# Kernel optimization log

Hardware: AMD Instinct MI355X
Metric: run time of the kernel (lower is better)

## Reference

```python
import jax, jax.numpy as jnp
import numpy as np

# Module hyperparams (from init_kwargs)
VX, VY = 0.16, 0.16
PC_RANGE = (0.0, -39.68, -3.0, 69.12, 39.68, 1.0)
X_OFFSET = VX / 2 + PC_RANGE[0]
Y_OFFSET = VY / 2 + PC_RANGE[1]
X_L = int((PC_RANGE[3] - PC_RANGE[0]) / VX)  # 432
Y_L = int((PC_RANGE[4] - PC_RANGE[1]) / VY)  # 496
IN_CH, OUT_CH = 9, 64
BN_EPS = 1e-3
P, N_MAX, B = 40000, 32, 4


def setup_inputs() -> dict:
    key = jax.random.key(0)
    k1, k2, k3 = jax.random.split(key, 3)
    pillars = jax.random.normal(k1, (P, N_MAX, 4), dtype=jnp.float32)
    # Unique (per batch) pillar coordinates so the scatter is well-defined.
    rng = np.random.default_rng(0)
    per = P // B
    rows = []
    for b in range(B):
        lin = rng.choice(Y_L * X_L, size=per, replace=False)
        ys, xs = lin // X_L, lin % X_L
        rows.append(np.stack([np.full(per, b, np.int32), xs.astype(np.int32), ys.astype(np.int32)], axis=1))
    coors_batch = jnp.asarray(np.concatenate(rows, axis=0))  # (P,3): [b, x, y]
    npoints_per_pillar = jax.random.randint(k2, (P,), 1, N_MAX + 1, dtype=jnp.int32)
    # Learned params: 1x1 Conv1d weight (no bias) + BN affine
    W = jax.random.normal(k3, (OUT_CH, IN_CH), dtype=jnp.float32) * 0.1
    gamma = jnp.ones((OUT_CH,), dtype=jnp.float32)
    beta = jnp.zeros((OUT_CH,), dtype=jnp.float32)
    return {"pillars": pillars, "coors_batch": coors_batch,
            "npoints_per_pillar": npoints_per_pillar,
            "W": W, "gamma": gamma, "beta": beta, "batch_size": B}


def reference(pillars, coors_batch, npoints_per_pillar, W, gamma, beta, batch_size):
    npts = npoints_per_pillar.astype(pillars.dtype)
    # offset of each point from pillar mean (xyz)
    center = jnp.sum(pillars[:, :, :3], axis=1, keepdims=True) / npts[:, None, None]
    offset_pt_center = pillars[:, :, :3] - center                      # (P,N,3)
    cx = coors_batch[:, None, 1:2].astype(pillars.dtype) * VX + X_OFFSET
    cy = coors_batch[:, None, 2:3].astype(pillars.dtype) * VY + Y_OFFSET
    x_off = pillars[:, :, :1] - cx                                     # (P,N,1)
    y_off = pillars[:, :, 1:2] - cy                                    # (P,N,1)
    features = jnp.concatenate([pillars, offset_pt_center, x_off, y_off], axis=-1)  # (P,N,9)
    mask = (jnp.arange(N_MAX)[None, :] < npoints_per_pillar[:, None]).astype(features.dtype)
    features = features * mask[:, :, None]
    # 1x1 Conv1d == per-point channel mix -> (P, C_out, N)
    x = jnp.einsum('pnc,oc->pon', features, W)
    # BatchNorm1d (training-mode stats over pillar and point dims, biased var)
    mean = jnp.mean(x, axis=(0, 2))
    var = jnp.var(x, axis=(0, 2))
    x = gamma[None, :, None] * (x - mean[None, :, None]) * jax.lax.rsqrt(var[None, :, None] + BN_EPS) + beta[None, :, None]
    x = jax.nn.relu(x)
    pooled = jnp.max(x, axis=-1)                                       # (P, C_out)
    # Single vectorized scatter into BEV canvas: (B, Y, X, C) then -> (B, C, Y, X)
    canvas = jnp.zeros((batch_size, Y_L, X_L, OUT_CH), dtype=jnp.float32)
    canvas = canvas.at[coors_batch[:, 0], coors_batch[:, 2], coors_batch[:, 1]].set(pooled)
    return jnp.transpose(canvas, (0, 3, 1, 2))
```

## Files before the change

kernel.cpp:

```cpp
#include <hip/hip_runtime.h>
#include <math.h>

#define P_TOT 40000
#define NMAX 32
#define BATCH 4
#define YL 496
#define XL 432
#define CIN 9
#define COUT 64
#define NTRI 45
#define PN_F 1280000.0f

#define MAP_ELEMS (BATCH * YL * XL)
#define MAP_BYTES (MAP_ELEMS * 4)
#define STATS_OFF MAP_BYTES
#define SCALE_OFF (STATS_OFF + 256)
#define SHIFT_OFF (SCALE_OFF + 256)
#define POOLED_OFF (SHIFT_OFF + 256)

#define STATS_BLOCKS 256

__global__ __launch_bounds__(256) void k_init(int* __restrict__ map,
                                              float* __restrict__ stats) {
    int i = blockIdx.x * 256 + threadIdx.x;
    if (i < MAP_ELEMS) map[i] = -1;
    if (i < 54) stats[i] = 0.0f;
}

__global__ __launch_bounds__(256) void k_stats(const float4* __restrict__ pillars,
                                               const int* __restrict__ coors,
                                               const int* __restrict__ npp,
                                               int* __restrict__ map,
                                               float* __restrict__ stats) {
    const int wave = threadIdx.x >> 6;
    const int lane = threadIdx.x & 63;
    const int half = lane >> 5;
    const int n = lane & 31;
    const int gw = blockIdx.x * 4 + wave;
    const int totalWaves = STATS_BLOCKS * 4;

    float s1[CIN];
    float s2[NTRI];
#pragma unroll
    for (int i = 0; i < CIN; i++) s1[i] = 0.0f;
#pragma unroll
    for (int i = 0; i < NTRI; i++) s2[i] = 0.0f;

    for (int p0 = gw * 2; p0 < P_TOT; p0 += totalWaves * 2) {
        int p = p0 + half;
        float4 q = pillars[(size_t)p * NMAX + n];

        float sx = q.x, sy = q.y, sz = q.z;
#pragma unroll
        for (int off = 1; off < 32; off <<= 1) {
            sx += __shfl_xor(sx, off, 32);
            sy += __shfl_xor(sy, off, 32);
            sz += __shfl_xor(sz, off, 32);
        }
        int npts = npp[p];
        float fn = (float)npts;
        float mx = sx / fn, my = sy / fn, mz = sz / fn;

        int xi = coors[p * 3 + 1];
        int yi = coors[p * 3 + 2];
        if (n == 0) {
            int b = coors[p * 3 + 0];
            map[(b * YL + yi) * XL + xi] = p;
        }
        float cx = (float)xi * 0.16f + 0.08f;
        float cy = (float)yi * 0.16f + (-39.6f);

        float msk = (n < npts) ? 1.0f : 0.0f;
        float f[CIN];
        f[0] = q.x * msk; f[1] = q.y * msk; f[2] = q.z * msk; f[3] = q.w * msk;
        f[4] = (q.x - mx) * msk; f[5] = (q.y - my) * msk; f[6] = (q.z - mz) * msk;
        f[7] = (q.x - cx) * msk; f[8] = (q.y - cy) * msk;

        int k = 0;
#pragma unroll
        for (int a = 0; a < CIN; a++) {
            s1[a] += f[a];
#pragma unroll
            for (int c = a; c < CIN; c++) s2[k++] += f[a] * f[c];
        }
    }

#pragma unroll
    for (int i = 0; i < CIN; i++) {
        float v = s1[i];
        for (int off = 1; off < 64; off <<= 1) v += __shfl_xor(v, off, 64);
        s1[i] = v;
    }
#pragma unroll
    for (int i = 0; i < NTRI; i++) {
        float v = s2[i];
        for (int off = 1; off < 64; off <<= 1) v += __shfl_xor(v, off, 64);
        s2[i] = v;
    }

    __shared__ float red[4][54];
    if (lane == 0) {
#pragma unroll
        for (int i = 0; i < CIN; i++) red[wave][i] = s1[i];
#pragma unroll
        for (int i = 0; i < NTRI; i++) red[wave][CIN + i] = s2[i];
    }
    __syncthreads();
    if (threadIdx.x < 54) {
        float v = red[0][threadIdx.x] + red[1][threadIdx.x] +
                  red[2][threadIdx.x] + red[3][threadIdx.x];
        atomicAdd(&stats[threadIdx.x], v);
    }
}

__global__ void k_finalize(const float* __restrict__ W,
                           const float* __restrict__ gamma,
                           const float* __restrict__ beta,
                           const float* __restrict__ stats,
                           float* __restrict__ scale,
                           float* __restrict__ shift) {
    int o = threadIdx.x;
    float w[CIN];
#pragma unroll
    for (int c = 0; c < CIN; c++) w[c] = W[o * CIN + c];

    const float invPN = 1.0f / PN_F;
    float mu = 0.0f;
#pragma unroll
    for (int c = 0; c < CIN; c++) mu += w[c] * (stats[c] * invPN);

    float ex2 = 0.0f;
    int k = 0;
#pragma unroll
    for (int a = 0; a < CIN; a++) {
#pragma unroll
        for (int c = a; c < CIN; c++) {
            float Mv = stats[CIN + k] * invPN;
            float t = w[a] * w[c] * Mv;
            ex2 += (a == c) ? t : 2.0f * t;
            k++;
        }
    }
    float var = ex2 - mu * mu;
    float sc = gamma[o] * rsqrtf(var + 1e-3f);
    scale[o] = sc;
    shift[o] = beta[o] - mu * sc;
}

__global__ __launch_bounds__(256) void k_pool(const float4* __restrict__ pillars,
                                              const int* __restrict__ coors,
                                              const int* __restrict__ npp,
                                              const float* __restrict__ W,
                                              const float* __restrict__ scale,
                                              const float* __restrict__ shift,
                                              float* __restrict__ pooled) {
    __shared__ float fsh[4][NMAX][CIN];
    int w = threadIdx.x >> 6;
    int lane = threadIdx.x & 63;
    int p = blockIdx.x * 4 + w;
    int n = lane & 31;

    float4 q = pillars[(size_t)p * NMAX + n];
    float sx = q.x, sy = q.y, sz = q.z;
#pragma unroll
    for (int off = 1; off < 32; off <<= 1) {
        sx += __shfl_xor(sx, off, 32);
        sy += __shfl_xor(sy, off, 32);
        sz += __shfl_xor(sz, off, 32);
    }
    int npts = npp[p];
    float fn = (float)npts;
    float mx = sx / fn, my = sy / fn, mz = sz / fn;
    int xi = coors[p * 3 + 1];
    int yi = coors[p * 3 + 2];
    float cx = (float)xi * 0.16f + 0.08f;
    float cy = (float)yi * 0.16f + (-39.6f);

    if (lane < 32) {
        bool valid = (n < npts);
        fsh[w][n][0] = valid ? q.x : 0.0f;
        fsh[w][n][1] = valid ? q.y : 0.0f;
        fsh[w][n][2] = valid ? q.z : 0.0f;
        fsh[w][n][3] = valid ? q.w : 0.0f;
        fsh[w][n][4] = valid ? (q.x - mx) : 0.0f;
        fsh[w][n][5] = valid ? (q.y - my) : 0.0f;
        fsh[w][n][6] = valid ? (q.z - mz) : 0.0f;
        fsh[w][n][7] = valid ? (q.x - cx) : 0.0f;
        fsh[w][n][8] = valid ? (q.y - cy) : 0.0f;
    }
    __syncthreads();

    float wv[CIN];
#pragma unroll
    for (int c = 0; c < CIN; c++) wv[c] = W[lane * CIN + c];
    float sc = scale[lane];
    float sh = shift[lane];

    float m = -INFINITY;
#pragma unroll 4
    for (int nn = 0; nn < NMAX; nn++) {
        float d = 0.0f;
#pragma unroll
        for (int c = 0; c < CIN; c++) d += wv[c] * fsh[w][nn][c];
        m = fmaxf(m, sc * d + sh);
    }
    pooled[(size_t)p * COUT + lane] = fmaxf(m, 0.0f);
}

__global__ __launch_bounds__(256) void k_scatter(const int* __restrict__ map,
                                                 const float* __restrict__ pooled,
                                                 float* __restrict__ out) {
    int i = blockIdx.x * 256 + threadIdx.x;
    if (i >= BATCH * YL * (XL / 4)) return;
    int x4 = i % (XL / 4);
    int r = i / (XL / 4);
    int y = r % YL;
    int b = r / YL;

    const int4 pid = *(const int4*)(map + (size_t)(b * YL + y) * XL + x4 * 4);
    size_t obase = ((size_t)(b * COUT) * YL + y) * XL + (size_t)x4 * 4;
    const size_t cstride = (size_t)YL * XL;

    const float4 zero = make_float4(0.f, 0.f, 0.f, 0.f);
#pragma unroll 4
    for (int c4 = 0; c4 < COUT / 4; c4++) {
        float4 r0 = zero, r1 = zero, r2 = zero, r3 = zero;
        if (pid.x >= 0) r0 = *(const float4*)(pooled + (size_t)pid.x * COUT + c4 * 4);
        if (pid.y >= 0) r1 = *(const float4*)(pooled + (size_t)pid.y * COUT + c4 * 4);
        if (pid.z >= 0) r2 = *(const float4*)(pooled + (size_t)pid.z * COUT + c4 * 4);
        if (pid.w >= 0) r3 = *(const float4*)(pooled + (size_t)pid.w * COUT + c4 * 4);
        float* o0 = out + obase + (size_t)(c4 * 4) * cstride;
        *(float4*)(o0)               = make_float4(r0.x, r1.x, r2.x, r3.x);
        *(float4*)(o0 + cstride)     = make_float4(r0.y, r1.y, r2.y, r3.y);
        *(float4*)(o0 + 2 * cstride) = make_float4(r0.z, r1.z, r2.z, r3.z);
        *(float4*)(o0 + 3 * cstride) = make_float4(r0.w, r1.w, r2.w, r3.w);
    }
}

extern "C" void kernel_launch(void* const* d_in, const int* in_sizes, int n_in,
                              void* d_out, int out_size, void* d_ws, size_t ws_size,
                              hipStream_t stream) {
    const float4* pillars = (const float4*)d_in[0];
    const int* coors = (const int*)d_in[1];
    const int* npp = (const int*)d_in[2];
    const float* W = (const float*)d_in[3];
    const float* gamma = (const float*)d_in[4];
    const float* beta = (const float*)d_in[5];
    float* out = (float*)d_out;

    char* ws = (char*)d_ws;
    int* map = (int*)(ws);
    float* stats = (float*)(ws + STATS_OFF);
    float* scale = (float*)(ws + SCALE_OFF);
    float* shift = (float*)(ws + SHIFT_OFF);
    float* pooled = (float*)(ws + POOLED_OFF);

    k_init<<<(MAP_ELEMS + 255) / 256, 256, 0, stream>>>(map, stats);
    k_stats<<<STATS_BLOCKS, 256, 0, stream>>>(pillars, coors, npp, map, stats);
    k_finalize<<<1, 64, 0, stream>>>(W, gamma, beta, stats, scale, shift);
    k_pool<<<P_TOT / 4, 256, 0, stream>>>(pillars, coors, npp, W, scale, shift, pooled);
    k_scatter<<<(BATCH * YL * (XL / 4) + 255) / 256, 256, 0, stream>>>(map, pooled, out);
}
```

Before: 318.6 us.

## Fuse all stages into one cooperative persistent kernel with grid syncs

```diff
diff --git a/kernel.cpp b/kernel.cpp
--- a/kernel.cpp
+++ b/kernel.cpp
@@ -1,5 +1,8 @@
 #include <hip/hip_runtime.h>
+#include <hip/hip_cooperative_groups.h>
 #include <math.h>
+
+namespace cg = cooperative_groups;
 
 #define P_TOT 40000
 #define NMAX 32
@@ -18,222 +21,229 @@
 #define SHIFT_OFF (SCALE_OFF + 256)
 #define POOLED_OFF (SHIFT_OFF + 256)
 
-#define STATS_BLOCKS 256
-
-__global__ __launch_bounds__(256) void k_init(int* __restrict__ map,
-                                              float* __restrict__ stats) {
-    int i = blockIdx.x * 256 + threadIdx.x;
-    if (i < MAP_ELEMS) map[i] = -1;
-    if (i < 54) stats[i] = 0.0f;
-}
-
-__global__ __launch_bounds__(256) void k_stats(const float4* __restrict__ pillars,
-                                               const int* __restrict__ coors,
-                                               const int* __restrict__ npp,
-                                               int* __restrict__ map,
-                                               float* __restrict__ stats) {
-    const int wave = threadIdx.x >> 6;
-    const int lane = threadIdx.x & 63;
-    const int half = lane >> 5;
-    const int n = lane & 31;
-    const int gw = blockIdx.x * 4 + wave;
-    const int totalWaves = STATS_BLOCKS * 4;
-
-    float s1[CIN];
-    float s2[NTRI];
-#pragma unroll
-    for (int i = 0; i < CIN; i++) s1[i] = 0.0f;
-#pragma unroll
-    for (int i = 0; i < NTRI; i++) s2[i] = 0.0f;
-
-    for (int p0 = gw * 2; p0 < P_TOT; p0 += totalWaves * 2) {
-        int p = p0 + half;
-        float4 q = pillars[(size_t)p * NMAX + n];
-
-        float sx = q.x, sy = q.y, sz = q.z;
-#pragma unroll
-        for (int off = 1; off < 32; off <<= 1) {
-            sx += __shfl_xor(sx, off, 32);
-            sy += __shfl_xor(sy, off, 32);
-            sz += __shfl_xor(sz, off, 32);
-        }
-        int npts = npp[p];
-        float fn = (float)npts;
-        float mx = sx / fn, my = sy / fn, mz = sz / fn;
-
-        int xi = coors[p * 3 + 1];
-        int yi = coors[p * 3 + 2];
-        if (n == 0) {
-            int b = coors[p * 3 + 0];
-            map[(b * YL + yi) * XL + xi] = p;
-        }
-        float cx = (float)xi * 0.16f + 0.08f;
-        float cy = (float)yi * 0.16f + (-39.6f);
-
-        float msk = (n < npts) ? 1.0f : 0.0f;
-        float f[CIN];
-        f[0] = q.x * msk; f[1] = q.y * msk; f[2] = q.z * msk; f[3] = q.w * msk;
-        f[4] = (q.x - mx) * msk; f[5] = (q.y - my) * msk; f[6] = (q.z - mz) * msk;
-        f[7] = (q.x - cx) * msk; f[8] = (q.y - cy) * msk;
-
+#define GRID_MAX 1024
+#define NCELL4 (BATCH * YL * (XL / 4))
+
+__global__ __launch_bounds__(256, 4) void k_fused(
+        const float4* __restrict__ pillars,
+        const int* __restrict__ coors,
+        const int* __restrict__ npp,
+        const float* __restrict__ W,
+        const float* __restrict__ gamma,
+        const float* __restrict__ beta,
+        int* __restrict__ map,
+        float* __restrict__ stats,
+        float* __restrict__ scale,
+        float* __restrict__ shift,
+        float* __restrict__ pooled,
+        float* __restrict__ out,
+        int nblocks) {
+    cg::grid_group grid = cg::this_grid();
+    const int tid = threadIdx.x;
+    const int gtid = blockIdx.x * 256 + tid;
+    const int nthreads = nblocks * 256;
+    const int wave = tid >> 6;
+    const int lane = tid & 63;
+
+    __shared__ float red[4][54];
+    __shared__ float fsh[4][NMAX][CIN];
+
+    {
+        int4* m4 = (int4*)map;
+        const int4 neg1 = make_int4(-1, -1, -1, -1);
+        for (int i = gtid; i < MAP_ELEMS / 4; i += nthreads) m4[i] = neg1;
+        if (gtid < 54) stats[gtid] = 0.0f;
+    }
+    grid.sync();
+
+    {
+        const int half = lane >> 5;
+        const int n = lane & 31;
+        const int gw = blockIdx.x * 4 + wave;
+        const int totalWaves = nblocks * 4;
+
+        float s1[CIN];
+        float s2[NTRI];
+#pragma unroll
+        for (int i = 0; i < CIN; i++) s1[i] = 0.0f;
+#pragma unroll
+        for (int i = 0; i < NTRI; i++) s2[i] = 0.0f;
+
+        for (int p0 = gw * 2; p0 < P_TOT; p0 += totalWaves * 2) {
+            int p = p0 + half;
+            float4 q = pillars[(size_t)p * NMAX + n];
+
+            float sx = q.x, sy = q.y, sz = q.z;
+#pragma unroll
+            for (int off = 1; off < 32; off <<= 1) {
+                sx += __shfl_xor(sx, off, 32);
+                sy += __shfl_xor(sy, off, 32);
+                sz += __shfl_xor(sz, off, 32);
+            }
+            int npts = npp[p];
+            float fn = (float)npts;
+            float mx = sx / fn, my = sy / fn, mz = sz / fn;
+
+            int xi = coors[p * 3 + 1];
+            int yi = coors[p * 3 + 2];
+            if (n == 0) {
+                int b = coors[p * 3 + 0];
+                map[(b * YL + yi) * XL + xi] = p;
+            }
+            float cx = (float)xi * 0.16f + 0.08f;
+            float cy = (float)yi * 0.16f + (-39.6f);
+
+            float msk = (n < npts) ? 1.0f : 0.0f;
+            float f[CIN];
+            f[0] = q.x * msk; f[1] = q.y * msk; f[2] = q.z * msk; f[3] = q.w * msk;
+            f[4] = (q.x - mx) * msk; f[5] = (q.y - my) * msk; f[6] = (q.z - mz) * msk;
+            f[7] = (q.x - cx) * msk; f[8] = (q.y - cy) * msk;
+
+            int k = 0;
+#pragma unroll
+            for (int a = 0; a < CIN; a++) {
+                s1[a] += f[a];
+#pragma unroll
+                for (int c = a; c < CIN; c++) s2[k++] += f[a] * f[c];
+            }
+        }
+
+#pragma unroll
+        for (int i = 0; i < CIN; i++) {
+            float v = s1[i];
+            for (int off = 1; off < 64; off <<= 1) v += __shfl_xor(v, off, 64);
+            s1[i] = v;
+        }
+#pragma unroll
+        for (int i = 0; i < NTRI; i++) {
+            float v = s2[i];
+            for (int off = 1; off < 64; off <<= 1) v += __shfl_xor(v, off, 64);
+            s2[i] = v;
+        }
+        if (lane == 0) {
+#pragma unroll
+            for (int i = 0; i < CIN; i++) red[wave][i] = s1[i];
+#pragma unroll
+            for (int i = 0; i < NTRI; i++) red[wave][CIN + i] = s2[i];
+        }
+        __syncthreads();
+        if (tid < 54) {
+            float v = red[0][tid] + red[1][tid] + red[2][tid] + red[3][tid];
+            atomicAdd(&stats[tid], v);
+        }
+    }
+    grid.sync();
+
+    if (blockIdx.x == 0 && tid < COUT) {
+        int o = tid;
+        float w[CIN];
+#pragma unroll
+        for (int c = 0; c < CIN; c++) w[c] = W[o * CIN + c];
+
+        const float invPN = 1.0f / PN_F;
+        float mu = 0.0f;
+#pragma unroll
+        for (int c = 0; c < CIN; c++) mu += w[c] * (stats[c] * invPN);
+
+        float ex2 = 0.0f;
         int k = 0;
 #pragma unroll
         for (int a = 0; a < CIN; a++) {
-            s1[a] += f[a];
-#pragma unroll
-            for (int c = a; c < CIN; c++) s2[k++] += f[a] * f[c];
-        }
-    }
-
-#pragma unroll
-    for (int i = 0; i < CIN; i++) {
-        float v = s1[i];
-        for (int off = 1; off < 64; off <<= 1) v += __shfl_xor(v, off, 64);
-        s1[i] = v;
-    }
-#pragma unroll
-    for (int i = 0; i < NTRI; i++) {
-        float v = s2[i];
-        for (int off = 1; off < 64; off <<= 1) v += __shfl_xor(v, off, 64);
-        s2[i] = v;
-    }
-
-    __shared__ float red[4][54];
-    if (lane == 0) {
-#pragma unroll
-        for (int i = 0; i < CIN; i++) red[wave][i] = s1[i];
-#pragma unroll
-        for (int i = 0; i < NTRI; i++) red[wave][CIN + i] = s2[i];
-    }
-    __syncthreads();
-    if (threadIdx.x < 54) {
-        float v = red[0][threadIdx.x] + red[1][threadIdx.x] +
-                  red[2][threadIdx.x] + red[3][threadIdx.x];
-        atomicAdd(&stats[threadIdx.x], v);
-    }
-}
-
-__global__ void k_finalize(const float* __restrict__ W,
-                           const float* __restrict__ gamma,
-                           const float* __restrict__ beta,
-                           const float* __restrict__ stats,
-                           float* __restrict__ scale,
-                           float* __restrict__ shift) {
-    int o = threadIdx.x;
-    float w[CIN];
-#pragma unroll
-    for (int c = 0; c < CIN; c++) w[c] = W[o * CIN + c];
-
-    const float invPN = 1.0f / PN_F;
-    float mu = 0.0f;
-#pragma unroll
-    for (int c = 0; c < CIN; c++) mu += w[c] * (stats[c] * invPN);
-
-    float ex2 = 0.0f;
-    int k = 0;
-#pragma unroll
-    for (int a = 0; a < CIN; a++) {
-#pragma unroll
-        for (int c = a; c < CIN; c++) {
-            float Mv = stats[CIN + k] * invPN;
-            float t = w[a] * w[c] * Mv;
-            ex2 += (a == c) ? t : 2.0f * t;
-            k++;
-        }
-    }
-    float var = ex2 - mu * mu;
-    float sc = gamma[o] * rsqrtf(var + 1e-3f);
-    scale[o] = sc;
-    shift[o] = beta[o] - mu * sc;
-}
-
-__global__ __launch_bounds__(256) void k_pool(const float4* __restrict__ pillars,
-                                              const int* __restrict__ coors,
-                                              const int* __restrict__ npp,
-                                              const float* __restrict__ W,
-                                              const float* __restrict__ scale,
-                                              const float* __restrict__ shift,
-                                              float* __restrict__ pooled) {
-    __shared__ float fsh[4][NMAX][CIN];
-    int w = threadIdx.x >> 6;
-    int lane = threadIdx.x & 63;
-    int p = blockIdx.x * 4 + w;
-    int n = lane & 31;
-
-    float4 q = pillars[(size_t)p * NMAX + n];
-    float sx = q.x, sy = q.y, sz = q.z;
-#pragma unroll
-    for (int off = 1; off < 32; off <<= 1) {
-        sx += __shfl_xor(sx, off, 32);
-        sy += __shfl_xor(sy, off, 32);
-        sz += __shfl_xor(sz, off, 32);
-    }
-    int npts = npp[p];
-    float fn = (float)npts;
-    float mx = sx / fn, my = sy / fn, mz = sz / fn;
-    int xi = coors[p * 3 + 1];
-    int yi = coors[p * 3 + 2];
-    float cx = (float)xi * 0.16f + 0.08f;
-    float cy = (float)yi * 0.16f + (-39.6f);
-
-    if (lane < 32) {
-        bool valid = (n < npts);
-        fsh[w][n][0] = valid ? q.x : 0.0f;
-        fsh[w][n][1] = valid ? q.y : 0.0f;
-        fsh[w][n][2] = valid ? q.z : 0.0f;
-        fsh[w][n][3] = valid ? q.w : 0.0f;
-        fsh[w][n][4] = valid ? (q.x - mx) : 0.0f;
-        fsh[w][n][5] = valid ? (q.y - my) : 0.0f;
-        fsh[w][n][6] = valid ? (q.z - mz) : 0.0f;
-        fsh[w][n][7] = valid ? (q.x - cx) : 0.0f;
-        fsh[w][n][8] = valid ? (q.y - cy) : 0.0f;
-    }
-    __syncthreads();
-
-    float wv[CIN];
-#pragma unroll
-    for (int c = 0; c < CIN; c++) wv[c] = W[lane * CIN + c];
-    float sc = scale[lane];
-    float sh = shift[lane];
-
-    float m = -INFINITY;
+#pragma unroll
+            for (int c = a; c < CIN; c++) {
+                float Mv = stats[CIN + k] * invPN;
+                float t = w[a] * w[c] * Mv;
+                ex2 += (a == c) ? t : 2.0f * t;
+                k++;
+            }
+        }
+        float var = ex2 - mu * mu;
+        float sc = gamma[o] * rsqrtf(var + 1e-3f);
+        scale[o] = sc;
+        shift[o] = beta[o] - mu * sc;
+    }
+    grid.sync();
+
+    {
+        float wv[CIN];
+#pragma unroll
+        for (int c = 0; c < CIN; c++) wv[c] = W[lane * CIN + c];
+        float sc = scale[lane];
+        float sh = shift[lane];
+        const int n = lane & 31;
+
+        for (int pb = blockIdx.x * 4; pb < P_TOT; pb += nblocks * 4) {
+            int p = pb + wave;
+            float4 q = pillars[(size_t)p * NMAX + n];
+            float sx = q.x, sy = q.y, sz = q.z;
+#pragma unroll
+            for (int off = 1; off < 32; off <<= 1) {
+                sx += __shfl_xor(sx, off, 32);
+                sy += __shfl_xor(sy, off, 32);
+                sz += __shfl_xor(sz, off, 32);
+            }
+            int npts = npp[p];
+            float fn = (float)npts;
+            float mx = sx / fn, my = sy / fn, mz = sz / fn;
+            int xi = coors[p * 3 + 1];
+            int yi = coors[p * 3 + 2];
+            float cx = (float)xi * 0.16f + 0.08f;
+            float cy = (float)yi * 0.16f + (-39.6f);
+
+            __syncthreads();
+            if (lane < 32) {
+                bool valid = (n < npts);
+                fsh[wave][n][0] = valid ? q.x : 0.0f;
+                fsh[wave][n][1] = valid ? q.y : 0.0f;
+                fsh[wave][n][2] = valid ? q.z : 0.0f;
+                fsh[wave][n][3] = valid ? q.w : 0.0f;
+                fsh[wave][n][4] = valid ? (q.x - mx) : 0.0f;
+                fsh[wave][n][5] = valid ? (q.y - my) : 0.0f;
+                fsh[wave][n][6] = valid ? (q.z - mz) : 0.0f;
+                fsh[wave][n][7] = valid ? (q.x - cx) : 0.0f;
+                fsh[wave][n][8] = valid ? (q.y - cy) : 0.0f;
+            }
+            __syncthreads();
+
+            float m = -INFINITY;
 #pragma unroll 4
-    for (int nn = 0; nn < NMAX; nn++) {
-        float d = 0.0f;
-#pragma unroll
-        for (int c = 0; c < CIN; c++) d += wv[c] * fsh[w][nn][c];
-        m = fmaxf(m, sc * d + sh);
-    }
-    pooled[(size_t)p * COUT + lane] = fmaxf(m, 0.0f);
-}
-
-__global__ __launch_bounds__(256) void k_scatter(const int* __restrict__ map,
-                                                 const float* __restrict__ pooled,
-                                                 float* __restrict__ out) {
-    int i = blockIdx.x * 256 + threadIdx.x;
-    if (i >= BATCH * YL * (XL / 4)) return;
-    int x4 = i % (XL / 4);
-    int r = i / (XL / 4);
-    int y = r % YL;
-    int b = r / YL;
-
-    const int4 pid = *(const int4*)(map + (size_t)(b * YL + y) * XL + x4 * 4);
-    size_t obase = ((size_t)(b * COUT) * YL + y) * XL + (size_t)x4 * 4;
-    const size_t cstride = (size_t)YL * XL;
-
-    const float4 zero = make_float4(0.f, 0.f, 0.f, 0.f);
+            for (int nn = 0; nn < NMAX; nn++) {
+                float d = 0.0f;
+#pragma unroll
+                for (int c = 0; c < CIN; c++) d += wv[c] * fsh[wave][nn][c];
+                m = fmaxf(m, sc * d + sh);
+            }
+            pooled[(size_t)p * COUT + lane] = fmaxf(m, 0.0f);
+        }
+    }
+    grid.sync();
+
+    {
+        const size_t cstride = (size_t)YL * XL;
+        const float4 zero = make_float4(0.f, 0.f, 0.f, 0.f);
+        for (int i = gtid; i < NCELL4; i += nthreads) {
+            int x4 = i % (XL / 4);
+            int r = i / (XL / 4);
+            int y = r % YL;
+            int b = r / YL;
+
+            const int4 pid = *(const int4*)(map + (size_t)(b * YL + y) * XL + x4 * 4);
+            size_t obase = ((size_t)(b * COUT) * YL + y) * XL + (size_t)x4 * 4;
+
 #pragma unroll 4
-    for (int c4 = 0; c4 < COUT / 4; c4++) {
-        float4 r0 = zero, r1 = zero, r2 = zero, r3 = zero;
-        if (pid.x >= 0) r0 = *(const float4*)(pooled + (size_t)pid.x * COUT + c4 * 4);
-        if (pid.y >= 0) r1 = *(const float4*)(pooled + (size_t)pid.y * COUT + c4 * 4);
-        if (pid.z >= 0) r2 = *(const float4*)(pooled + (size_t)pid.z * COUT + c4 * 4);
-        if (pid.w >= 0) r3 = *(const float4*)(pooled + (size_t)pid.w * COUT + c4 * 4);
-        float* o0 = out + obase + (size_t)(c4 * 4) * cstride;
-        *(float4*)(o0)               = make_float4(r0.x, r1.x, r2.x, r3.x);
-        *(float4*)(o0 + cstride)     = make_float4(r0.y, r1.y, r2.y, r3.y);
-        *(float4*)(o0 + 2 * cstride) = make_float4(r0.z, r1.z, r2.z, r3.z);
-        *(float4*)(o0 + 3 * cstride) = make_float4(r0.w, r1.w, r2.w, r3.w);
+            for (int c4 = 0; c4 < COUT / 4; c4++) {
+                float4 r0 = zero, r1 = zero, r2 = zero, r3 = zero;
+                if (pid.x >= 0) r0 = *(const float4*)(pooled + (size_t)pid.x * COUT + c4 * 4);
+                if (pid.y >= 0) r1 = *(const float4*)(pooled + (size_t)pid.y * COUT + c4 * 4);
+                if (pid.z >= 0) r2 = *(const float4*)(pooled + (size_t)pid.z * COUT + c4 * 4);
+                if (pid.w >= 0) r3 = *(const float4*)(pooled + (size_t)pid.w * COUT + c4 * 4);
+                float* o0 = out + obase + (size_t)(c4 * 4) * cstride;
+                *(float4*)(o0)               = make_float4(r0.x, r1.x, r2.x, r3.x);
+                *(float4*)(o0 + cstride)     = make_float4(r0.y, r1.y, r2.y, r3.y);
+                *(float4*)(o0 + 2 * cstride) = make_float4(r0.z, r1.z, r2.z, r3.z);
+                *(float4*)(o0 + 3 * cstride) = make_float4(r0.w, r1.w, r2.w, r3.w);
+            }
+        }
     }
 }
 
@@ -255,9 +265,16 @@
     float* shift = (float*)(ws + SHIFT_OFF);
     float* pooled = (float*)(ws + POOLED_OFF);
 
-    k_init<<<(MAP_ELEMS + 255) / 256, 256, 0, stream>>>(map, stats);
-    k_stats<<<STATS_BLOCKS, 256, 0, stream>>>(pillars, coors, npp, map, stats);
-    k_finalize<<<1, 64, 0, stream>>>(W, gamma, beta, stats, scale, shift);
-    k_pool<<<P_TOT / 4, 256, 0, stream>>>(pillars, coors, npp, W, scale, shift, pooled);
-    k_scatter<<<(BATCH * YL * (XL / 4) + 255) / 256, 256, 0, stream>>>(map, pooled, out);
+    int maxBlocksPerCU = 4;
+    hipOccupancyMaxActiveBlocksPerMultiprocessor(&maxBlocksPerCU, k_fused, 256, 0);
+    int nblocks = maxBlocksPerCU * 256;
+    if (nblocks > GRID_MAX) nblocks = GRID_MAX;
+    if (nblocks < 256) nblocks = 256;
+
+    void* args[] = {(void*)&pillars, (void*)&coors, (void*)&npp, (void*)&W,
+                    (void*)&gamma, (void*)&beta, (void*)&map, (void*)&stats,
+                    (void*)&scale, (void*)&shift, (void*)&pooled, (void*)&out,
+                    (void*)&nblocks};
+    hipLaunchCooperativeKernel((const void*)k_fused, dim3(nblocks), dim3(256),
+                               args, 0, stream);
 }
```

New measurement: 528.8 us. +66.0%, slower.
